# Kernel optimization log

Measured on AMD Instinct MI355X. Metric: run time of the kernel, lower is better.

## Reference

```python
import jax, jax.numpy as jnp
import numpy as np

N_NODES = 50000
N_EDGES = 800000
N_GRAPHS = 64


def graph_conv(x, edge_index, w_rel, b_rel, w_root):
    # PyG GraphConv with aggr='add':
    #   out = lin_rel(sum_{j in N(i)} x_j) + lin_root(x_i)
    src, dst = edge_index[0], edge_index[1]
    agg = jax.ops.segment_sum(x[src], dst, num_segments=x.shape[0])  # [N, d_in]
    return agg @ w_rel + b_rel + x @ w_root  # [N, d_out]


def scatter_mean(x, batch, num_segments):
    s = jax.ops.segment_sum(x, batch, num_segments=num_segments)
    cnt = jax.ops.segment_sum(jnp.ones((x.shape[0],), x.dtype), batch,
                              num_segments=num_segments)
    return s / jnp.maximum(cnt, 1.0)[:, None]


def setup_inputs() -> dict:
    key = jax.random.key(0)
    ks = jax.random.split(key, 8)
    d_feat, d_hid, d_out = 128, 128, 128
    x = jax.random.normal(ks[0], (N_NODES, d_feat), dtype=jnp.float32)
    edge_index = jax.random.randint(ks[1], (2, N_EDGES), 0, N_NODES, dtype=jnp.int64)
    batch = jnp.sort(jax.random.randint(ks[2], (N_NODES,), 0, N_GRAPHS, dtype=jnp.int64))

    def glorot(k, shape):
        fan_in = shape[0]
        return jax.random.normal(k, shape, dtype=jnp.float32) / np.sqrt(fan_in)

    return {
        "x": x,
        "edge_index": edge_index,
        "batch": batch,
        "w_rel1": glorot(ks[3], (d_feat, d_hid)),
        "b_rel1": jnp.zeros((d_hid,), jnp.float32),
        "w_root1": glorot(ks[4], (d_feat, d_hid)),
        "w_rel2": glorot(ks[5], (d_hid, 2 * d_hid)),
        "b_rel2": jnp.zeros((2 * d_hid,), jnp.float32),
        "w_root2": glorot(ks[6], (d_hid, 2 * d_hid)),
        "w_rel3": glorot(ks[7], (2 * d_hid, d_out)),
        "b_rel3": jnp.zeros((d_out,), jnp.float32),
        "w_root3": glorot(jax.random.fold_in(key, 99), (2 * d_hid, d_out)),
    }


def reference(x, edge_index, batch,
              w_rel1, b_rel1, w_root1,
              w_rel2, b_rel2, w_root2,
              w_rel3, b_rel3, w_root3):
    h = jax.nn.elu(graph_conv(x, edge_index, w_rel1, b_rel1, w_root1))
    h = jax.nn.elu(graph_conv(h, edge_index, w_rel2, b_rel2, w_root2))
    h = jax.nn.elu(graph_conv(h, edge_index, w_rel3, b_rel3, w_root3))
    return scatter_mean(h, batch, N_GRAPHS)  # [num_graphs, n_out]
```

## Files before the change

### kernel.cpp

```cpp
#include <hip/hip_runtime.h>
#include <math.h>

#define NN 50000
#define NNP 50048
#define NE 800000
#define NG 64
#define NBK 196
#define ECH 4082
#define TOTH (NBK * NBK)
#define NBH 151
#define SBLK 6890
#define SWORK (NN * 32 + 163840)

typedef __attribute__((ext_vector_type(8))) __bf16 bf16x8;
typedef __attribute__((ext_vector_type(4))) float f32x4;

__device__ inline unsigned short f2bf(float f) {
    unsigned int u = __float_as_uint(f);
    u += 0x7fffu + ((u >> 16) & 1u);
    return (unsigned short)(u >> 16);
}
__device__ inline float bflo(unsigned int v) { return __uint_as_float(v << 16); }
__device__ inline float bfhi(unsigned int v) { return __uint_as_float(v & 0xffff0000u); }
__device__ inline float bfs(unsigned short v) { return __uint_as_float((unsigned int)v << 16); }

#define GLD_LDS16(g, l)                                                          \
    __builtin_amdgcn_global_load_lds(                                            \
        (const __attribute__((address_space(1))) unsigned int*)(g),              \
        (__attribute__((address_space(3))) unsigned int*)(l), 16, 0, 0)

__global__ __launch_bounds__(256) void front_k(const float* __restrict__ x,
                                               const float* __restrict__ wr1,
                                               const float* __restrict__ wo1,
                                               const float* __restrict__ wr2,
                                               const float* __restrict__ wo2,
                                               const float* __restrict__ wr3,
                                               const float* __restrict__ wo3,
                                               const int* __restrict__ edst,
                                               const int* __restrict__ batch,
                                               unsigned short* __restrict__ xb,
                                               unsigned short* __restrict__ W1T,
                                               unsigned short* __restrict__ W2T,
                                               unsigned short* __restrict__ W3T,
                                               int* __restrict__ H,
                                               int* __restrict__ bounds,
                                               float* __restrict__ outp) {
    const int b = blockIdx.x, t = threadIdx.x;
    if (b < SBLK) {
        int id = b * 256 + t;
        if (id < NN * 32) {
            float4 v = ((const float4*)x)[id];
            unsigned int p0 = ((unsigned int)f2bf(v.y) << 16) | f2bf(v.x);
            unsigned int p1 = ((unsigned int)f2bf(v.w) << 16) | f2bf(v.z);
            ((uint2*)xb)[id] = make_uint2(p0, p1);
            return;
        }
        int w = id - NN * 32;
        if (w < 32768) {
            int n = w >> 8, k = w & 255;
            W1T[w] = f2bf((k < 128) ? wr1[k * 128 + n] : wo1[(k - 128) * 128 + n]);
        } else if (w < 98304) {
            int j = w - 32768; int n = j >> 8, k = j & 255;
            W2T[j] = f2bf((k < 128) ? wr2[k * 256 + n] : wo2[(k - 128) * 256 + n]);
        } else if (w < 163840) {
            int j = w - 98304; int n = j >> 8, k = j & 255;
            W3T[j] = f2bf((n < 128) ? wr3[k * 128 + n] : wo3[k * 128 + (n - 128)]);
        }
        return;
    }
    if (b < SBLK + NBK) {
        __shared__ int h[NBK];
        int k = b - SBLK;
        if (t < NBK) h[t] = 0;
        __syncthreads();
        int e0 = k * ECH, e1 = min(NE, e0 + ECH);
        for (int e = e0 + t; e < e1; e += 256) atomicAdd(&h[edst[e] >> 8], 1);
        __syncthreads();
        if (t < NBK) H[t * NBK + k] = h[t];
        return;
    }
    if (t <= NG) {
        int g = t, lo = 0, hi = NN;
        while (lo < hi) { int mid = (lo + hi) >> 1; if (batch[mid] < g) lo = mid + 1; else hi = mid; }
        bounds[g] = lo;
    }
    for (int i = t; i < NG * 128; i += 256) outp[i] = 0.f;
}

__global__ __launch_bounds__(256) void hsum_k(const int* __restrict__ H,
                                              int* __restrict__ hb) {
    int i = blockIdx.x * 256 + threadIdx.x;
    int v = (i < TOTH) ? H[i] : 0;
    for (int off = 32; off; off >>= 1) v += __shfl_xor(v, off, 64);
    __shared__ int ws[4];
    if ((threadIdx.x & 63) == 0) ws[threadIdx.x >> 6] = v;
    __syncthreads();
    if (threadIdx.x == 0) hb[blockIdx.x] = ws[0] + ws[1] + ws[2] + ws[3];
}

__global__ __launch_bounds__(256) void happly_k(const int* __restrict__ H,
                                                const int* __restrict__ hb,
                                                int* __restrict__ S) {
    __shared__ int s[256], ws[4], choff;
    const int t = threadIdx.x, c = blockIdx.x;
    {
        int v = (t < c) ? hb[t] : 0;
        for (int off = 32; off; off >>= 1) v += __shfl_xor(v, off, 64);
        if ((t & 63) == 0) ws[t >> 6] = v;
        __syncthreads();
        if (t == 0) choff = ws[0] + ws[1] + ws[2] + ws[3];
        __syncthreads();
    }
    int i = c * 256 + t;
    int v = (i < TOTH) ? H[i] : 0;
    s[t] = v; __syncthreads();
    for (int off = 1; off < 256; off <<= 1) {
        int u = (t >= off) ? s[t - off] : 0;
        __syncthreads(); s[t] += u; __syncthreads();
    }
    if (i < TOTH) S[i] = choff + s[t] - v;
}

__global__ __launch_bounds__(256) void scatter_k(const int* __restrict__ src,
                                                 const int* __restrict__ dst,
                                                 const int* __restrict__ S,
                                                 int* __restrict__ tmp) {
    __shared__ int cur[NBK];
    int t = threadIdx.x, k = blockIdx.x;
    if (t < NBK) cur[t] = S[t * NBK + k];
    __syncthreads();
    int e0 = k * ECH, e1 = min(NE, e0 + ECH);
    for (int e = e0 + t; e < e1; e += 256) {
        int d = dst[e];
        int p = atomicAdd(&cur[d >> 8], 1);
        tmp[p] = ((d & 255) << 16) | src[e];
    }
}

__global__ __launch_bounds__(256) void csr_k(const int* __restrict__ tmp,
                                             const int* __restrict__ S,
                                             int* __restrict__ rowptr,
                                             int* __restrict__ colsrc) {
    __shared__ int hist[256], off[256], cur[256];
    int t = threadIdx.x, b = blockIdx.x;
    int base = S[b * NBK];
    int next = (b < NBK - 1) ? S[(b + 1) * NBK] : NE;
    int cntb = next - base;
    hist[t] = 0;
    __syncthreads();
    for (int i = t; i < cntb; i += 256) atomicAdd(&hist[tmp[base + i] >> 16], 1);
    __syncthreads();
    int v = hist[t];
    off[t] = v; __syncthreads();
    for (int o = 1; o < 256; o <<= 1) {
        int u = (t >= o) ? off[t - o] : 0;
        __syncthreads(); off[t] += u; __syncthreads();
    }
    int excl = off[t] - v;
    int node = b * 256 + t;
    if (node <= NN) rowptr[node] = base + excl;
    cur[t] = excl;
    __syncthreads();
    for (int i = t; i < cntb; i += 256) {
        int e = tmp[base + i];
        int p = atomicAdd(&cur[e >> 16], 1);
        colsrc[base + p] = e & 0xffff;
    }
}

__global__ __launch_bounds__(256) void aggb_k(const unsigned short* __restrict__ feat,
                                              const int* __restrict__ rowptr,
                                              const int* __restrict__ colsrc,
                                              unsigned short* __restrict__ outp) {
    const int node = __builtin_amdgcn_readfirstlane((int)(blockIdx.x * 4 + (threadIdx.x >> 6)));
    const int lane = threadIdx.x & 63;
    const int half = lane >> 5, l32 = lane & 31;
    const int beg = rowptr[node], end = rowptr[node + 1];
    float a0 = 0.f, a1 = 0.f, a2 = 0.f, a3 = 0.f;
    int e = beg;
    for (; e + 16 <= end; e += 16) {
        int c[8]; uint2 v[8];
#pragma unroll
        for (int i = 0; i < 8; ++i) c[i] = colsrc[e + 2 * i + half];
#pragma unroll
        for (int i = 0; i < 8; ++i)
            v[i] = *(const uint2*)&feat[(size_t)c[i] * 128 + l32 * 4];
#pragma unroll
        for (int i = 0; i < 8; ++i) {
            a0 += bflo(v[i].x); a1 += bfhi(v[i].x);
            a2 += bflo(v[i].y); a3 += bfhi(v[i].y);
        }
    }
    for (; e + 4 <= end; e += 4) {
        int c[2]; uint2 v[2];
#pragma unroll
        for (int i = 0; i < 2; ++i) c[i] = colsrc[e + 2 * i + half];
#pragma unroll
        for (int i = 0; i < 2; ++i)
            v[i] = *(const uint2*)&feat[(size_t)c[i] * 128 + l32 * 4];
#pragma unroll
        for (int i = 0; i < 2; ++i) {
            a0 += bflo(v[i].x); a1 += bfhi(v[i].x);
            a2 += bflo(v[i].y); a3 += bfhi(v[i].y);
        }
    }
    if (e + 2 <= end) {
        int c = colsrc[e + half];
        uint2 v = *(const uint2*)&feat[(size_t)c * 128 + l32 * 4];
        a0 += bflo(v.x); a1 += bfhi(v.x); a2 += bflo(v.y); a3 += bfhi(v.y);
        e += 2;
    }
    if (e < end && half == 0) {
        int c = colsrc[e];
        uint2 v = *(const uint2*)&feat[(size_t)c * 128 + l32 * 4];
        a0 += bflo(v.x); a1 += bfhi(v.x); a2 += bflo(v.y); a3 += bfhi(v.y);
    }
    a0 += __shfl_xor(a0, 32, 64);
    a1 += __shfl_xor(a1, 32, 64);
    a2 += __shfl_xor(a2, 32, 64);
    a3 += __shfl_xor(a3, 32, 64);
    if (half == 0) {
        unsigned int p0 = ((unsigned int)f2bf(a1) << 16) | f2bf(a0);
        unsigned int p1 = ((unsigned int)f2bf(a3) << 16) | f2bf(a2);
        *(uint2*)&outp[(size_t)node * 128 + l32 * 4] = make_uint2(p0, p1);
    }
}

__global__ __launch_bounds__(256) void aggf_k(const unsigned short* __restrict__ y,
                                              const unsigned short* __restrict__ rr,
                                              const float* __restrict__ b3,
                                              const int* __restrict__ rowptr,
                                              const int* __restrict__ colsrc,
                                              unsigned short* __restrict__ outp) {
    const int node = __builtin_amdgcn_readfirstlane((int)(blockIdx.x * 4 + (threadIdx.x >> 6)));
    const int lane = threadIdx.x & 63;
    const int half = lane >> 5, l32 = lane & 31;
    const int beg = rowptr[node], end = rowptr[node + 1];
    float a0 = 0.f, a1 = 0.f, a2 = 0.f, a3 = 0.f;
    int e = beg;
    for (; e + 16 <= end; e += 16) {
        int c[8]; uint2 v[8];
#pragma unroll
        for (int i = 0; i < 8; ++i) c[i] = colsrc[e + 2 * i + half];
#pragma unroll
        for (int i = 0; i < 8; ++i)
            v[i] = *(const uint2*)&y[(size_t)c[i] * 128 + l32 * 4];
#pragma unroll
        for (int i = 0; i < 8; ++i) {
            a0 += bflo(v[i].x); a1 += bfhi(v[i].x);
            a2 += bflo(v[i].y); a3 += bfhi(v[i].y);
        }
    }
    for (; e + 4 <= end; e += 4) {
        int c[2]; uint2 v[2];
#pragma unroll
        for (int i = 0; i < 2; ++i) c[i] = colsrc[e + 2 * i + half];
#pragma unroll
        for (int i = 0; i < 2; ++i)
            v[i] = *(const uint2*)&y[(size_t)c[i] * 128 + l32 * 4];
#pragma unroll
        for (int i = 0; i < 2; ++i) {
            a0 += bflo(v[i].x); a1 += bfhi(v[i].x);
            a2 += bflo(v[i].y); a3 += bfhi(v[i].y);
        }
    }
    if (e + 2 <= end) {
        int c = colsrc[e + half];
        uint2 v = *(const uint2*)&y[(size_t)c * 128 + l32 * 4];
        a0 += bflo(v.x); a1 += bfhi(v.x); a2 += bflo(v.y); a3 += bfhi(v.y);
        e += 2;
    }
    if (e < end && half == 0) {
        int c = colsrc[e];
        uint2 v = *(const uint2*)&y[(size_t)c * 128 + l32 * 4];
        a0 += bflo(v.x); a1 += bfhi(v.x); a2 += bflo(v.y); a3 += bfhi(v.y);
    }
    a0 += __shfl_xor(a0, 32, 64);
    a1 += __shfl_xor(a1, 32, 64);
    a2 += __shfl_xor(a2, 32, 64);
    a3 += __shfl_xor(a3, 32, 64);
    if (half == 0) {
        uint2 rv = *(const uint2*)&rr[(size_t)node * 128 + l32 * 4];
        float4 bb = *(const float4*)&b3[l32 * 4];
        float v0 = a0 + bflo(rv.x) + bb.x;
        float v1 = a1 + bfhi(rv.x) + bb.y;
        float v2 = a2 + bflo(rv.y) + bb.z;
        float v3 = a3 + bfhi(rv.y) + bb.w;
        v0 = v0 > 0.f ? v0 : (__expf(v0) - 1.f);
        v1 = v1 > 0.f ? v1 : (__expf(v1) - 1.f);
        v2 = v2 > 0.f ? v2 : (__expf(v2) - 1.f);
        v3 = v3 > 0.f ? v3 : (__expf(v3) - 1.f);
        unsigned int p0 = ((unsigned int)f2bf(v1) << 16) | f2bf(v0);
        unsigned int p1 = ((unsigned int)f2bf(v3) << 16) | f2bf(v2);
        *(uint2*)&outp[(size_t)node * 128 + l32 * 4] = make_uint2(p0, p1);
    }
}

template <int MT, int KA, int N, bool TWO, bool BIAS, bool ELU>
__global__ __launch_bounds__(256) void gemm_k(const unsigned short* __restrict__ A1,
                                              const unsigned short* __restrict__ A2,
                                              const unsigned short* __restrict__ WT,
                                              const float* __restrict__ bias,
                                              unsigned short* __restrict__ Cout) {
    constexpr int KTOT = TWO ? 2 * KA : KA;
    constexpr int NSTEP = KTOT / 32;
    constexpr int MI = MT / 32;
    constexpr int LA = MT / 64;
    constexpr int LB = N / 64;
    __shared__ __attribute__((aligned(16))) unsigned short As[2][MT * 32];
    __shared__ __attribute__((aligned(16))) unsigned short Bs[2][N * 32];
    const int t = threadIdx.x;
    const int wv = t >> 6, lane = t & 63;
    const int qd = lane >> 4, l16 = lane & 15;
    const int m0 = blockIdx.x * MT;
    const int mh = (wv & 1) * (MT / 2), nh = (wv >> 1) * 64;
    const int srow = lane >> 2;
    const int skk  = (lane & 3) * 8;

    f32x4 acc[MI][4] = {};

    auto stage = [&](int k0, int buf) {
        const unsigned short* Abase = (TWO && k0 >= KA) ? (A2 + (k0 - KA)) : (A1 + k0);
#pragma unroll
        for (int i = 0; i < LA; ++i) {
            int chunk = wv * LA + i;
            const unsigned short* g = Abase + (size_t)(m0 + chunk * 16 + srow) * KA + skk;
            GLD_LDS16(g, &As[buf][chunk * 512]);
        }
        const unsigned short* Wbase = WT + k0;
#pragma unroll
        for (int i = 0; i < LB; ++i) {
            int chunk = wv * LB + i;
            const unsigned short* g = Wbase + (size_t)(chunk * 16 + srow) * KTOT + skk;
            GLD_LDS16(g, &Bs[buf][chunk * 512]);
        }
    };

    stage(0, 0);
    for (int s = 0; s < NSTEP; ++s) {
        const int cur = s & 1;
        if (s + 1 < NSTEP) {
            stage((s + 1) * 32, cur ^ 1);
            asm volatile("s_waitcnt vmcnt(%0)" :: "i"(LA + LB) : "memory");
        } else {
            asm volatile("s_waitcnt vmcnt(0)" ::: "memory");
        }
        __builtin_amdgcn_s_barrier();
        asm volatile("" ::: "memory");
        bf16x8 af[MI], bfr[4];
#pragma unroll
        for (int mi = 0; mi < MI; ++mi)
            af[mi] = *(const bf16x8*)&As[cur][(mh + mi * 16 + l16) * 32 + qd * 8];
#pragma unroll
        for (int ni = 0; ni < 4; ++ni)
            bfr[ni] = *(const bf16x8*)&Bs[cur][(nh + ni * 16 + l16) * 32 + qd * 8];
#pragma unroll
        for (int mi = 0; mi < MI; ++mi)
#pragma unroll
            for (int ni = 0; ni < 4; ++ni)
                acc[mi][ni] = __builtin_amdgcn_mfma_f32_16x16x32_bf16(
                    af[mi], bfr[ni], acc[mi][ni], 0, 0, 0);
        asm volatile("" ::: "memory");
        __builtin_amdgcn_s_barrier();
    }

#pragma unroll
    for (int mi = 0; mi < MI; ++mi)
#pragma unroll
        for (int ni = 0; ni < 4; ++ni)
#pragma unroll
            for (int r = 0; r < 4; ++r) {
                int mm = m0 + mh + mi * 16 + qd * 4 + r;
                if (mm < NN) {
                    int nn = nh + ni * 16 + l16;
                    float v = acc[mi][ni][r];
                    if (BIAS) v += bias[nn];
                    if (ELU) v = v > 0.f ? v : (__expf(v) - 1.f);
                    Cout[(size_t)mm * N + nn] = f2bf(v);
                }
            }
}

template <int KA, bool TWO, bool BIAS, bool ELU, bool SPLIT>
__global__ __launch_bounds__(256) void gemm256_k(const unsigned short* __restrict__ A1,
                                                 const unsigned short* __restrict__ A2,
                                                 const unsigned short* __restrict__ WT,
                                                 const float* __restrict__ bias,
                                                 unsigned short* __restrict__ Cout,
                                                 unsigned short* __restrict__ Cout2) {
    constexpr int KTOT = TWO ? 2 * KA : KA;
    constexpr int NSTEP = KTOT / 32;
    __shared__ __attribute__((aligned(16))) unsigned short As[2][64 * 32];
    __shared__ __attribute__((aligned(16))) unsigned short Bs[2][256 * 32];
    const int t = threadIdx.x;
    const int wv = t >> 6, lane = t & 63;
    const int qd = lane >> 4, l16 = lane & 15;
    const int m0 = blockIdx.x * 64;
    const int srow = lane >> 2;
    const int skk  = (lane & 3) * 8;

    f32x4 acc[4][4] = {};

    auto stage = [&](int k0, int buf) {
        const unsigned short* Abase = (TWO && k0 >= KA) ? (A2 + (k0 - KA)) : (A1 + k0);
        {
            const unsigned short* g = Abase + (size_t)(m0 + wv * 16 + srow) * KA + skk;
            GLD_LDS16(g, &As[buf][wv * 512]);
        }
        const unsigned short* Wbase = WT + k0;
#pragma unroll
        for (int i = 0; i < 4; ++i) {
            int chunk = wv * 4 + i;
            const unsigned short* g = Wbase + (size_t)(chunk * 16 + srow) * KTOT + skk;
            GLD_LDS16(g, &Bs[buf][chunk * 512]);
        }
    };

    stage(0, 0);
    for (int s = 0; s < NSTEP; ++s) {
        const int cur = s & 1;
        if (s + 1 < NSTEP) {
            stage((s + 1) * 32, cur ^ 1);
            asm volatile("s_waitcnt vmcnt(%0)" :: "i"(5) : "memory");
        } else {
            asm volatile("s_waitcnt vmcnt(0)" ::: "memory");
        }
        __builtin_amdgcn_s_barrier();
        asm volatile("" ::: "memory");
        bf16x8 af[4], bfr[4];
#pragma unroll
        for (int mi = 0; mi < 4; ++mi)
            af[mi] = *(const bf16x8*)&As[cur][(mi * 16 + l16) * 32 + qd * 8];
#pragma unroll
        for (int ni = 0; ni < 4; ++ni)
            bfr[ni] = *(const bf16x8*)&Bs[cur][(wv * 64 + ni * 16 + l16) * 32 + qd * 8];
#pragma unroll
        for (int mi = 0; mi < 4; ++mi)
#pragma unroll
            for (int ni = 0; ni < 4; ++ni)
                acc[mi][ni] = __builtin_amdgcn_mfma_f32_16x16x32_bf16(
                    af[mi], bfr[ni], acc[mi][ni], 0, 0, 0);
        asm volatile("" ::: "memory");
        __builtin_amdgcn_s_barrier();
    }

#pragma unroll
    for (int mi = 0; mi < 4; ++mi)
#pragma unroll
        for (int ni = 0; ni < 4; ++ni)
#pragma unroll
            for (int r = 0; r < 4; ++r) {
                int mm = m0 + mi * 16 + qd * 4 + r;
                if (mm < NN) {
                    int nn = wv * 64 + ni * 16 + l16;
                    float v = acc[mi][ni][r];
                    if (BIAS) v += bias[nn];
                    if (ELU) v = v > 0.f ? v : (__expf(v) - 1.f);
                    unsigned short b = f2bf(v);
                    if (SPLIT) {
                        unsigned short* dst = (nn < 128) ? Cout : Cout2;
                        dst[(size_t)mm * 128 + (nn & 127)] = b;
                    } else {
                        Cout[(size_t)mm * 256 + nn] = b;
                    }
                }
            }
}

__global__ __launch_bounds__(256) void sum_k(const unsigned short* __restrict__ vals,
                                             const int* __restrict__ batch,
                                             float* __restrict__ outsum) {
    const int CH = 25;
    int wv = threadIdx.x >> 6, lane = threadIdx.x & 63;
    int n0 = (blockIdx.x * 4 + wv) * CH;
    int g = batch[n0];
    float ax = 0.f, ay = 0.f;
    for (int i = 0; i < CH; ++i) {
        int n = n0 + i;
        int gn = batch[n];
        if (gn != g) {
            unsafeAtomicAdd(&outsum[(size_t)g * 128 + lane * 2], ax);
            unsafeAtomicAdd(&outsum[(size_t)g * 128 + lane * 2 + 1], ay);
            ax = 0.f; ay = 0.f; g = gn;
        }
        unsigned int v = *(const unsigned int*)&vals[(size_t)n * 128 + lane * 2];
        ax += bflo(v); ay += bfhi(v);
    }
    unsafeAtomicAdd(&outsum[(size_t)g * 128 + lane * 2], ax);
    unsafeAtomicAdd(&outsum[(size_t)g * 128 + lane * 2 + 1], ay);
}

__global__ void divide_k(const int* __restrict__ bounds, float* __restrict__ out) {
    int i = blockIdx.x * 256 + threadIdx.x;
    if (i < NG * 128) {
        int g = i >> 7;
        float c = (float)(bounds[g + 1] - bounds[g]);
        out[i] /= fmaxf(c, 1.f);
    }
}

extern "C" void kernel_launch(void* const* d_in, const int* in_sizes, int n_in,
                              void* d_out, int out_size, void* d_ws, size_t ws_size,
                              hipStream_t stream) {
    const float* x       = (const float*)d_in[0];
    const int*   ei      = (const int*)d_in[1];
    const int*   batch   = (const int*)d_in[2];
    const float* w_rel1  = (const float*)d_in[3];
    const float* b_rel1  = (const float*)d_in[4];
    const float* w_root1 = (const float*)d_in[5];
    const float* w_rel2  = (const float*)d_in[6];
    const float* b_rel2  = (const float*)d_in[7];
    const float* w_root2 = (const float*)d_in[8];
    const float* w_rel3  = (const float*)d_in[9];
    const float* b_rel3  = (const float*)d_in[10];
    const float* w_root3 = (const float*)d_in[11];
    const int* esrc = ei;
    const int* edst = ei + NE;

    unsigned short* Ab = (unsigned short*)d_ws;
    unsigned short* Bb = Ab + (size_t)NNP * 128;
    unsigned short* Cb = Bb + (size_t)NNP * 128;
    unsigned short* xb = Cb + (size_t)NNP * 256;
    unsigned short* W1T = xb + (size_t)NNP * 128;
    unsigned short* W2T = W1T + 128 * 256;
    unsigned short* W3T = W2T + 256 * 256;
    int* rowptr = (int*)(W3T + 256 * 256);
    int* colsrc = rowptr + (NN + 1);
    int* tmp    = colsrc + NE;
    int* H      = tmp + NE;
    int* S      = H + TOTH;
    int* hb     = S + TOTH;
    int* bounds = hb + 256;
    float* outp = (float*)d_out;

    front_k<<<SBLK + NBK + 1, 256, 0, stream>>>(
        x, w_rel1, w_root1, w_rel2, w_root2, w_rel3, w_root3, edst, batch,
        xb, W1T, W2T, W3T, H, bounds, outp);
    hsum_k<<<NBH, 256, 0, stream>>>(H, hb);
    happly_k<<<NBH, 256, 0, stream>>>(H, hb, S);
    scatter_k<<<NBK, 256, 0, stream>>>(esrc, edst, S, tmp);
    csr_k<<<NBK, 256, 0, stream>>>(tmp, S, rowptr, colsrc);

    aggb_k<<<NN / 4, 256, 0, stream>>>(xb, rowptr, colsrc, Ab);
    gemm_k<64, 128, 128, true, true, true>
        <<<NNP / 64, 256, 0, stream>>>(Ab, xb, W1T, b_rel1, Bb);

    aggb_k<<<NN / 4, 256, 0, stream>>>(Bb, rowptr, colsrc, Ab);
    gemm256_k<128, true, true, true, false>
        <<<NNP / 64, 256, 0, stream>>>(Ab, Bb, W2T, b_rel2, Cb, nullptr);

    gemm256_k<256, false, false, false, true>
        <<<NNP / 64, 256, 0, stream>>>(Cb, nullptr, W3T, nullptr, Ab, Bb);

    aggf_k<<<NN / 4, 256, 0, stream>>>(Ab, Bb, b_rel3, rowptr, colsrc, Cb);
    sum_k<<<NN / 100, 256, 0, stream>>>(Cb, batch, outp);
    divide_k<<<(NG * 128 + 255) / 256, 256, 0, stream>>>(bounds, outp);
}
```

Baseline: 299.4 us.

## Replace GEMM kernels with unified kernel staging B in swizzled LDS, A direct to registers

Result: no change. 305.1 us (+1.9%).

```diff
diff --git a/kernel.cpp b/kernel.cpp
--- a/kernel.cpp
+++ b/kernel.cpp
@@ -296,172 +296,100 @@
     }
 }
 
-template <int MT, int KA, int N, bool TWO, bool BIAS, bool ELU>
-__global__ __launch_bounds__(256) void gemm_k(const unsigned short* __restrict__ A1,
-                                              const unsigned short* __restrict__ A2,
-                                              const unsigned short* __restrict__ WT,
-                                              const float* __restrict__ bias,
-                                              unsigned short* __restrict__ Cout) {
-    constexpr int KTOT = TWO ? 2 * KA : KA;
-    constexpr int NSTEP = KTOT / 32;
-    constexpr int MI = MT / 32;
-    constexpr int LA = MT / 64;
-    constexpr int LB = N / 64;
-    __shared__ __attribute__((aligned(16))) unsigned short As[2][MT * 32];
-    __shared__ __attribute__((aligned(16))) unsigned short Bs[2][N * 32];
-    const int t = threadIdx.x;
-    const int wv = t >> 6, lane = t & 63;
-    const int qd = lane >> 4, l16 = lane & 15;
-    const int m0 = blockIdx.x * MT;
-    const int mh = (wv & 1) * (MT / 2), nh = (wv >> 1) * 64;
-    const int srow = lane >> 2;
-    const int skk  = (lane & 3) * 8;
-
-    f32x4 acc[MI][4] = {};
-
-    auto stage = [&](int k0, int buf) {
-        const unsigned short* Abase = (TWO && k0 >= KA) ? (A2 + (k0 - KA)) : (A1 + k0);
-#pragma unroll
-        for (int i = 0; i < LA; ++i) {
-            int chunk = wv * LA + i;
-            const unsigned short* g = Abase + (size_t)(m0 + chunk * 16 + srow) * KA + skk;
-            GLD_LDS16(g, &As[buf][chunk * 512]);
-        }
-        const unsigned short* Wbase = WT + k0;
-#pragma unroll
-        for (int i = 0; i < LB; ++i) {
-            int chunk = wv * LB + i;
-            const unsigned short* g = Wbase + (size_t)(chunk * 16 + srow) * KTOT + skk;
-            GLD_LDS16(g, &Bs[buf][chunk * 512]);
-        }
-    };
-
-    stage(0, 0);
-    for (int s = 0; s < NSTEP; ++s) {
-        const int cur = s & 1;
-        if (s + 1 < NSTEP) {
-            stage((s + 1) * 32, cur ^ 1);
-            asm volatile("s_waitcnt vmcnt(%0)" :: "i"(LA + LB) : "memory");
-        } else {
-            asm volatile("s_waitcnt vmcnt(0)" ::: "memory");
-        }
-        __builtin_amdgcn_s_barrier();
-        asm volatile("" ::: "memory");
-        bf16x8 af[MI], bfr[4];
-#pragma unroll
-        for (int mi = 0; mi < MI; ++mi)
-            af[mi] = *(const bf16x8*)&As[cur][(mh + mi * 16 + l16) * 32 + qd * 8];
-#pragma unroll
-        for (int ni = 0; ni < 4; ++ni)
-            bfr[ni] = *(const bf16x8*)&Bs[cur][(nh + ni * 16 + l16) * 32 + qd * 8];
-#pragma unroll
-        for (int mi = 0; mi < MI; ++mi)
-#pragma unroll
-            for (int ni = 0; ni < 4; ++ni)
-                acc[mi][ni] = __builtin_amdgcn_mfma_f32_16x16x32_bf16(
-                    af[mi], bfr[ni], acc[mi][ni], 0, 0, 0);
-        asm volatile("" ::: "memory");
-        __builtin_amdgcn_s_barrier();
-    }
-
-#pragma unroll
-    for (int mi = 0; mi < MI; ++mi)
-#pragma unroll
-        for (int ni = 0; ni < 4; ++ni)
-#pragma unroll
-            for (int r = 0; r < 4; ++r) {
-                int mm = m0 + mh + mi * 16 + qd * 4 + r;
-                if (mm < NN) {
-                    int nn = nh + ni * 16 + l16;
-                    float v = acc[mi][ni][r];
-                    if (BIAS) v += bias[nn];
-                    if (ELU) v = v > 0.f ? v : (__expf(v) - 1.f);
-                    Cout[(size_t)mm * N + nn] = f2bf(v);
-                }
-            }
-}
-
-template <int KA, bool TWO, bool BIAS, bool ELU, bool SPLIT>
-__global__ __launch_bounds__(256) void gemm256_k(const unsigned short* __restrict__ A1,
-                                                 const unsigned short* __restrict__ A2,
-                                                 const unsigned short* __restrict__ WT,
-                                                 const float* __restrict__ bias,
-                                                 unsigned short* __restrict__ Cout,
-                                                 unsigned short* __restrict__ Cout2) {
-    constexpr int KTOT = TWO ? 2 * KA : KA;
-    constexpr int NSTEP = KTOT / 32;
-    __shared__ __attribute__((aligned(16))) unsigned short As[2][64 * 32];
-    __shared__ __attribute__((aligned(16))) unsigned short Bs[2][256 * 32];
+template <bool TWO, int N, bool BIAS, bool ELU, bool SPLIT>
+__global__ __launch_bounds__(256) void gemmB_k(const unsigned short* __restrict__ A1,
+                                               const unsigned short* __restrict__ A2,
+                                               const unsigned short* __restrict__ WT,
+                                               const float* __restrict__ bias,
+                                               unsigned short* __restrict__ Cout,
+                                               unsigned short* __restrict__ Cout2) {
+    constexpr int AST = TWO ? 128 : 256;
+    constexpr int NH = N / 2;
+    constexpr int NI = NH / 16;
+    constexpr int SIT = N / 16;
+    __shared__ __attribute__((aligned(16))) unsigned short Bs[N * 128];
+
     const int t = threadIdx.x;
     const int wv = t >> 6, lane = t & 63;
     const int qd = lane >> 4, l16 = lane & 15;
     const int m0 = blockIdx.x * 64;
-    const int srow = lane >> 2;
-    const int skk  = (lane & 3) * 8;
-
-    f32x4 acc[4][4] = {};
-
-    auto stage = [&](int k0, int buf) {
-        const unsigned short* Abase = (TWO && k0 >= KA) ? (A2 + (k0 - KA)) : (A1 + k0);
-        {
-            const unsigned short* g = Abase + (size_t)(m0 + wv * 16 + srow) * KA + skk;
-            GLD_LDS16(g, &As[buf][wv * 512]);
-        }
-        const unsigned short* Wbase = WT + k0;
-#pragma unroll
-        for (int i = 0; i < 4; ++i) {
-            int chunk = wv * 4 + i;
-            const unsigned short* g = Wbase + (size_t)(chunk * 16 + srow) * KTOT + skk;
-            GLD_LDS16(g, &Bs[buf][chunk * 512]);
+    const int mrow = m0 + (wv >> 1) * 32 + l16;
+    const int nb = (wv & 1) * NH;
+    const int swz = (t & 15) ^ (t >> 4);
+
+    f32x4 acc[2][NI] = {};
+    bf16x8 av[2][2];
+
+    auto stageB = [&](int p) {
+#pragma unroll
+        for (int i = 0; i < SIT; ++i) {
+            int row = i * 16 + (t >> 4);
+            const unsigned short* g = WT + (size_t)row * 256 + p * 128 + swz * 8;
+            GLD_LDS16(g, &Bs[i * 2048 + t * 8]);
         }
     };
-
-    stage(0, 0);
-    for (int s = 0; s < NSTEP; ++s) {
-        const int cur = s & 1;
-        if (s + 1 < NSTEP) {
-            stage((s + 1) * 32, cur ^ 1);
-            asm volatile("s_waitcnt vmcnt(%0)" :: "i"(5) : "memory");
-        } else {
-            asm volatile("s_waitcnt vmcnt(0)" ::: "memory");
-        }
-        __builtin_amdgcn_s_barrier();
-        asm volatile("" ::: "memory");
-        bf16x8 af[4], bfr[4];
-#pragma unroll
-        for (int mi = 0; mi < 4; ++mi)
-            af[mi] = *(const bf16x8*)&As[cur][(mi * 16 + l16) * 32 + qd * 8];
-#pragma unroll
-        for (int ni = 0; ni < 4; ++ni)
-            bfr[ni] = *(const bf16x8*)&Bs[cur][(wv * 64 + ni * 16 + l16) * 32 + qd * 8];
-#pragma unroll
-        for (int mi = 0; mi < 4; ++mi)
-#pragma unroll
-            for (int ni = 0; ni < 4; ++ni)
+    auto loadA = [&](int ks, int d) {
+        const unsigned short* base = (TWO && ks >= 4) ? A2 : A1;
+        int kc = TWO ? ((ks & 3) * 32) : (ks * 32);
+        av[d][0] = *(const bf16x8*)&base[(size_t)mrow * AST + kc + qd * 8];
+        av[d][1] = *(const bf16x8*)&base[(size_t)(mrow + 16) * AST + kc + qd * 8];
+    };
+    auto kstep = [&](int ks, int d) {
+        int ksl = ks & 3;
+        bf16x8 bfr[NI];
+#pragma unroll
+        for (int ni = 0; ni < NI; ++ni) {
+            int row = nb + ni * 16 + l16;
+            int slot = (ksl * 4 + qd) ^ l16;
+            bfr[ni] = *(const bf16x8*)&Bs[row * 128 + slot * 8];
+        }
+#pragma unroll
+        for (int mi = 0; mi < 2; ++mi)
+#pragma unroll
+            for (int ni = 0; ni < NI; ++ni)
                 acc[mi][ni] = __builtin_amdgcn_mfma_f32_16x16x32_bf16(
-                    af[mi], bfr[ni], acc[mi][ni], 0, 0, 0);
-        asm volatile("" ::: "memory");
-        __builtin_amdgcn_s_barrier();
-    }
-
-#pragma unroll
-    for (int mi = 0; mi < 4; ++mi)
-#pragma unroll
-        for (int ni = 0; ni < 4; ++ni)
+                    av[d][mi], bfr[ni], acc[mi][ni], 0, 0, 0);
+    };
+
+    stageB(0);
+    asm volatile("" ::: "memory");
+    loadA(0, 0);
+    asm volatile("s_waitcnt vmcnt(2)" ::: "memory");
+    __builtin_amdgcn_s_barrier();
+    loadA(1, 1); kstep(0, 0);
+    loadA(2, 0); kstep(1, 1);
+    loadA(3, 1); kstep(2, 0);
+    kstep(3, 1);
+    asm volatile("s_waitcnt lgkmcnt(0)" ::: "memory");
+    __builtin_amdgcn_s_barrier();
+    stageB(1);
+    asm volatile("" ::: "memory");
+    loadA(4, 0);
+    asm volatile("s_waitcnt vmcnt(2)" ::: "memory");
+    __builtin_amdgcn_s_barrier();
+    loadA(5, 1); kstep(4, 0);
+    loadA(6, 0); kstep(5, 1);
+    loadA(7, 1); kstep(6, 0);
+    kstep(7, 1);
+
+#pragma unroll
+    for (int mi = 0; mi < 2; ++mi)
+#pragma unroll
+        for (int ni = 0; ni < NI; ++ni)
 #pragma unroll
             for (int r = 0; r < 4; ++r) {
-                int mm = m0 + mi * 16 + qd * 4 + r;
+                int mm = m0 + (wv >> 1) * 32 + mi * 16 + qd * 4 + r;
                 if (mm < NN) {
-                    int nn = wv * 64 + ni * 16 + l16;
+                    int nn = nb + ni * 16 + l16;
                     float v = acc[mi][ni][r];
                     if (BIAS) v += bias[nn];
                     if (ELU) v = v > 0.f ? v : (__expf(v) - 1.f);
-                    unsigned short b = f2bf(v);
+                    unsigned short bv = f2bf(v);
                     if (SPLIT) {
                         unsigned short* dst = (nn < 128) ? Cout : Cout2;
-                        dst[(size_t)mm * 128 + (nn & 127)] = b;
+                        dst[(size_t)mm * 128 + (nn & 127)] = bv;
                     } else {
-                        Cout[(size_t)mm * 256 + nn] = b;
+                        Cout[(size_t)mm * N + nn] = bv;
                     }
                 }
             }
@@ -542,14 +470,14 @@
     csr_k<<<NBK, 256, 0, stream>>>(tmp, S, rowptr, colsrc);
 
     aggb_k<<<NN / 4, 256, 0, stream>>>(xb, rowptr, colsrc, Ab);
-    gemm_k<64, 128, 128, true, true, true>
-        <<<NNP / 64, 256, 0, stream>>>(Ab, xb, W1T, b_rel1, Bb);
+    gemmB_k<true, 128, true, true, false>
+        <<<NNP / 64, 256, 0, stream>>>(Ab, xb, W1T, b_rel1, Bb, nullptr);
 
     aggb_k<<<NN / 4, 256, 0, stream>>>(Bb, rowptr, colsrc, Ab);
-    gemm256_k<128, true, true, true, false>
+    gemmB_k<true, 256, true, true, false>
         <<<NNP / 64, 256, 0, stream>>>(Ab, Bb, W2T, b_rel2, Cb, nullptr);
 
-    gemm256_k<256, false, false, false, true>
+    gemmB_k<false, 256, false, false, true>
         <<<NNP / 64, 256, 0, stream>>>(Cb, nullptr, W3T, nullptr, Ab, Bb);
 
     aggf_k<<<NN / 4, 256, 0, stream>>>(Ab, Bb, b_rel3, rowptr, colsrc, Cb);
```
